# Optimization experiments

Measured on AMD Instinct MI355X. Metric: run time of the kernel, lower is better.

## Reference

```python
import jax, jax.numpy as jnp
import numpy as np

NUM_Q_HEADS = 64
NUM_KV_HEADS = 8
HEAD_DIM = 64
HIDDEN = 2880
SLIDING_WINDOW = 128
ROPE_WAVELENGTH = 10000.0
NEG_INF = jnp.float32(-1e9)


def _rope(x, start_index=0):
    # x: (b, s, n, h). yarn with scaling_factor=1.0 == standard RoPE (split-half rotate).
    s, h = x.shape[1], x.shape[-1]
    inv_freq = 1.0 / (ROPE_WAVELENGTH ** (jnp.arange(0, h, 2, dtype=jnp.float32) / h))
    pos = jnp.arange(s, dtype=jnp.float32) + start_index
    freqs = pos[:, None] * inv_freq[None, :]  # (s, h/2)
    cos = jnp.concatenate([jnp.cos(freqs), jnp.cos(freqs)], axis=-1)[None, :, None, :]
    sin = jnp.concatenate([jnp.sin(freqs), jnp.sin(freqs)], axis=-1)[None, :, None, :]
    x1, x2 = jnp.split(x, 2, axis=-1)
    rot = jnp.concatenate([-x2, x1], axis=-1)
    return x * cos + rot * sin


def setup_inputs() -> dict:
    key = jax.random.key(0)
    ks = jax.random.split(key, 9)
    b, s = 1, 2048
    scale = 0.02
    hidden_states = jax.random.normal(ks[0], (b, s, HIDDEN), jnp.float32)
    Wq = jax.random.normal(ks[1], (HIDDEN, NUM_Q_HEADS, HEAD_DIM), jnp.float32) * scale
    Wk = jax.random.normal(ks[2], (HIDDEN, NUM_KV_HEADS, HEAD_DIM), jnp.float32) * scale
    Wv = jax.random.normal(ks[3], (HIDDEN, NUM_KV_HEADS, HEAD_DIM), jnp.float32) * scale
    Wo = jax.random.normal(ks[4], (NUM_Q_HEADS, HEAD_DIM, HIDDEN), jnp.float32) * scale
    bq = jnp.zeros((NUM_Q_HEADS, HEAD_DIM), jnp.float32)
    bk = jnp.zeros((NUM_KV_HEADS, HEAD_DIM), jnp.float32)
    bv = jnp.zeros((NUM_KV_HEADS, HEAD_DIM), jnp.float32)
    bo = jnp.zeros((HIDDEN,), jnp.float32)
    sinks = jax.random.normal(ks[5], (NUM_Q_HEADS,), jnp.float32) * 0.05
    attention_mask = jnp.tril(jnp.ones((s, s), bool))[None]  # causal, (b, q, k)
    return dict(hidden_states=hidden_states, Wq=Wq, bq=bq, Wk=Wk, bk=bk, Wv=Wv,
                bv=bv, Wo=Wo, bo=bo, sinks=sinks, attention_mask=attention_mask)


def reference(hidden_states, Wq, bq, Wk, bk, Wv, bv, Wo, bo, sinks, attention_mask):
    b, s, _ = hidden_states.shape
    inv_norm = 1.0 / np.sqrt(HEAD_DIM).astype(np.float32)
    # QKV projections (EinsumDense with bias)
    q = jnp.einsum('bqm,muh->bquh', hidden_states, Wq) + bq
    k = jnp.einsum('bkm,mvh->bkvh', hidden_states, Wk) + bk
    v = jnp.einsum('bkm,mvh->bkvh', hidden_states, Wv) + bv
    # rotary_dim == head_dim (even), so RoPE applies to the full head dim
    q = _rope(q)
    k = _rope(k)
    # GQA: repeat kv heads
    groups = NUM_Q_HEADS // NUM_KV_HEADS
    k = jnp.repeat(k, groups, axis=2)
    v = jnp.repeat(v, groups, axis=2)
    scores = jnp.einsum('bquh,bkuh->buqk', q, k) * inv_norm
    # sliding-window mask: keep kv_pos >= q_pos - window
    qpos = jnp.arange(s)
    swin = qpos[None, :] >= qpos[:, None] - SLIDING_WINDOW  # (q, k)
    scores = jnp.where(swin[None, None], scores, NEG_INF)
    scores = jnp.where(attention_mask[:, None], scores, NEG_INF)
    # sink-token logit per head appended as extra kv column
    sink = jnp.broadcast_to(sinks.reshape(1, NUM_Q_HEADS, 1, 1), (b, NUM_Q_HEADS, s, 1))
    logits = jnp.concatenate([scores, sink], axis=-1)
    m = jax.lax.stop_gradient(jnp.max(logits, axis=-1, keepdims=True))
    probs = jax.nn.softmax(logits - m, axis=-1)[..., :-1]  # drop sink column
    attn = jnp.einsum('buqk,bkuh->bquh', probs, v)
    return jnp.einsum('bquh,uhm->bqm', attn, Wo) + bo
```

## Files before the change

### kernel.cpp

```cpp
#include <hip/hip_runtime.h>
#include <cstdint>

typedef __attribute__((ext_vector_type(4))) float f32x4;
typedef __attribute__((ext_vector_type(8))) short bf16x8;

#define HIDDEN 2880
#define SEQ 2048
#define QKV_N 5120
#define WIN 128

__device__ __forceinline__ ushort f2bf(float f) {
  uint32_t u = __builtin_bit_cast(uint32_t, f);
  u += 0x7fff + ((u >> 16) & 1);
  return (ushort)(u >> 16);
}
__device__ __forceinline__ float bf2f(ushort h) {
  uint32_t u = ((uint32_t)h) << 16;
  return __builtin_bit_cast(float, u);
}

__global__ void conv_kernel(const float* __restrict__ in, ushort* __restrict__ out, int n) {
  int i = (blockIdx.x * blockDim.x + threadIdx.x) * 4;
  if (i >= n) return;
  float4 v = *(const float4*)(in + i);
  ushort4 o;
  o.x = f2bf(v.x); o.y = f2bf(v.y); o.z = f2bf(v.z); o.w = f2bf(v.w);
  *(ushort4*)(out + i) = o;
}

__global__ __launch_bounds__(256) void tconv_kernel(const float* __restrict__ in, ushort* __restrict__ out,
                                                    int R, int C, int out_ld, int out_row_off) {
  __shared__ float tile[32][33];
  int c0 = blockIdx.x * 32, r0 = blockIdx.y * 32;
  int tx = threadIdx.x & 31, ty = threadIdx.x >> 5;
#pragma unroll
  for (int i = 0; i < 32; i += 8)
    tile[ty + i][tx] = in[(size_t)(r0 + ty + i) * C + c0 + tx];
  __syncthreads();
#pragma unroll
  for (int i = 0; i < 32; i += 8)
    out[(size_t)(out_row_off + c0 + ty + i) * out_ld + r0 + tx] = f2bf(tile[tx][ty + i]);
}

__global__ void biascat_kernel(const float* __restrict__ bq, const float* __restrict__ bk,
                               const float* __restrict__ bv, float* __restrict__ out) {
  int i = blockIdx.x * blockDim.x + threadIdx.x;
  if (i >= QKV_N) return;
  float v = (i < 4096) ? bq[i] : (i < 4608) ? bk[i - 4096] : bv[i - 4608];
  out[i] = v;
}

__global__ void ropetab_kernel(float2* __restrict__ tab) {
  int i = blockIdx.x * blockDim.x + threadIdx.x;
  int s = i >> 5, d = i & 31;
  float inv = powf(10000.0f, -(float)d / 32.0f);
  float f = (float)s * inv;
  tab[i] = make_float2(cosf(f), sinf(f));
}

__global__ void rope_kernel(ushort* __restrict__ buf, const float2* __restrict__ tab, int width, int total) {
  int idx = blockIdx.x * blockDim.x + threadIdx.x;
  if (idx >= total) return;
  int s = idx / width;
  int rr = idx - s * width;
  int d = rr & 63;
  ushort* p = buf + (size_t)s * QKV_N + rr;
  float x = bf2f(*p);
  float partner = __shfl_xor(x, 32, 64);
  float2 cs = tab[(s << 5) + (d & 31)];
  float o = x * cs.x + ((d < 32) ? -partner : partner) * cs.y;
  *p = f2bf(o);
}

__global__ __launch_bounds__(256) void vt_kernel(const ushort* __restrict__ qkv, ushort* __restrict__ vt) {
  __shared__ ushort tile[64][80];
  int kv0 = blockIdx.x * 64, d0 = blockIdx.y * 64;
  int t = threadIdx.x;
#pragma unroll
  for (int p = 0; p < 2; ++p) {
    int lr = p * 32 + (t >> 3);
    *(bf16x8*)&tile[lr][(t & 7) * 8] =
        *(const bf16x8*)&qkv[(size_t)(kv0 + lr) * QKV_N + 4608 + d0 + (t & 7) * 8];
  }
  __syncthreads();
#pragma unroll
  for (int p = 0; p < 2; ++p) {
    int dl = p * 32 + (t >> 3);
    bf16x8 o;
#pragma unroll
    for (int jj = 0; jj < 8; ++jj) o[jj] = (short)tile[(t & 7) * 8 + jj][dl];
    *(bf16x8*)&vt[(size_t)(d0 + dl) * 2048 + kv0 + (t & 7) * 8] = o;
  }
}

template <bool OUT_BF16>
__global__ __launch_bounds__(256, 2) void gemm4w_kernel(
    const ushort* __restrict__ A, const ushort* __restrict__ Bt,
    const float* __restrict__ bias, void* __restrict__ Cv,
    int K, int lda, int ldb, int ldc) {
  constexpr int NFRAG = 5;
  constexpr int BHALF = 160 * 64;
  constexpr int BCHUNKS = 10;
  constexpr int BUFBYTES = 16384 + 2 * BHALF;
  __shared__ __align__(16) char ldsbuf[2 * BUFBYTES];

  const int cpx = gridDim.x >> 3;
  const int wg = ((int)blockIdx.x & 7) * cpx + ((int)blockIdx.x >> 3);
  const int mtile = wg & 15, ntile = wg >> 4;
  const int m0 = mtile * 128, n0 = ntile * 160;

  const int tid = threadIdx.x, wv = tid >> 6, l = tid & 63;
  const int wm = wv >> 1, wn = wv & 1;
  const int r = l & 15, g = l >> 4;

  const int c = l ^ ((l >> 3) & 3);
  const ushort* gA0 = A + (size_t)(m0 + (c >> 2)) * lda + (c & 3) * 8;
  const ushort* gB0 = Bt + (size_t)(n0 + (c >> 2)) * ldb + (c & 3) * 8;

  const int gsw = (g * 16) ^ (((r >> 1) & 3) << 4);
  const int aOff = (wm * 64 + r) * 64 + gsw;
  const int bOff = (wn * 80 + r) * 64 + gsw;

  auto sA = [&](int nb, int kg, int kh) {
#pragma unroll
    for (int j = 0; j < 2; ++j) {
      int cid = j * 4 + wv;
      __builtin_amdgcn_global_load_lds(
          (const __attribute__((address_space(1))) void*)(const void*)(gA0 + (size_t)cid * 16 * lda + kg),
          (__attribute__((address_space(3))) void*)&ldsbuf[nb * BUFBYTES + kh * 8192 + cid * 1024], 16, 0, 0);
    }
  };
  auto sB = [&](int nb, int kg, int kh) {
#pragma unroll
    for (int j = 0; j < 3; ++j) {
      int cid = j * 4 + wv;
      if (cid < BCHUNKS)
        __builtin_amdgcn_global_load_lds(
            (const __attribute__((address_space(1))) void*)(const void*)(gB0 + (size_t)cid * 16 * ldb + kg),
            (__attribute__((address_space(3))) void*)&ldsbuf[nb * BUFBYTES + 16384 + kh * BHALF + cid * 1024],
            16, 0, 0);
    }
  };

#define BAR() __builtin_amdgcn_s_barrier()
#define LGKM0()                                              \
  do {                                                       \
    asm volatile("s_waitcnt lgkmcnt(0)" ::: "memory");       \
    __builtin_amdgcn_sched_barrier(0);                       \
  } while (0)
#define WAITV0() asm volatile("s_waitcnt vmcnt(0)" ::: "memory")

  f32x4 acc[4][NFRAG] = {};
  const int nt = K >> 6;

  sA(0, 0, 0); sA(0, 32, 1); sB(0, 0, 0); sB(0, 32, 1);
  WAITV0();
  BAR();

  for (int t = 0; t < nt; ++t) {
    const int bufOff = (t & 1) * BUFBYTES;
    const int nb = (t & 1) ^ 1;
    if (t + 1 < nt) {
      const int kn = (t + 1) * 64;
      sA(nb, kn, 0); sA(nb, kn + 32, 1);
      sB(nb, kn, 0); sB(nb, kn + 32, 1);
    }
#pragma unroll
    for (int kh = 0; kh < 2; ++kh) {
      bf16x8 aq[4], bq[NFRAG];
#pragma unroll
      for (int nf = 0; nf < NFRAG; ++nf)
        bq[nf] = *(const bf16x8*)&ldsbuf[bufOff + 16384 + kh * BHALF + bOff + nf * 1024];
#pragma unroll
      for (int mi = 0; mi < 4; ++mi)
        aq[mi] = *(const bf16x8*)&ldsbuf[bufOff + kh * 8192 + aOff + mi * 1024];
      LGKM0();
      __builtin_amdgcn_s_setprio(1);
#pragma unroll
      for (int mi = 0; mi < 4; ++mi)
#pragma unroll
        for (int nf = 0; nf < NFRAG; ++nf)
          acc[mi][nf] = __builtin_amdgcn_mfma_f32_16x16x32_bf16(aq[mi], bq[nf], acc[mi][nf], 0, 0, 0);
      __builtin_amdgcn_s_setprio(0);
    }
    WAITV0();
    BAR();
  }

#pragma unroll
  for (int mf2 = 0; mf2 < 4; ++mf2) {
#pragma unroll
    for (int nf = 0; nf < NFRAG; ++nf) {
      int cc = n0 + wn * 80 + nf * 16 + r;
      float b = bias[cc];
#pragma unroll
      for (int j = 0; j < 4; ++j) {
        int rrow = m0 + wm * 64 + mf2 * 16 + g * 4 + j;
        float v = acc[mf2][nf][j] + b;
        if (OUT_BF16) ((ushort*)Cv)[(size_t)rrow * ldc + cc] = f2bf(v);
        else ((float*)Cv)[(size_t)rrow * ldc + cc] = v;
      }
    }
  }
#undef BAR
#undef LGKM0
#undef WAITV0
}

__global__ __launch_bounds__(512, 4) void attn_kernel(
    const ushort* __restrict__ qkv, const ushort* __restrict__ vt,
    const float* __restrict__ sinks, ushort* __restrict__ out) {
  __shared__ __align__(16) char lds[54272];
  const int kh = blockIdx.y;
  const int q0 = blockIdx.x * 32;
  const int kvw0 = q0 - 128;
  const int tid = threadIdx.x, w = tid >> 6, l = tid & 63;
  const int r = l & 15, g = l >> 4;
  const int h = kh * 8 + w;

  if (tid < 256) ((uint32_t*)(lds + 40960))[tid] = 0;

#pragma unroll
  for (int it = 0; it < 3; ++it) {
    int c = it * 512 + tid;
    if (c < 1280) {
      {
        int row = c >> 3, ch = c & 7;
        int kv = kvw0 + row;
        bf16x8 vv = {};
        if (kv >= 0) vv = *(const bf16x8*)&qkv[(size_t)kv * QKV_N + 4096 + kh * 64 + ch * 8];
        int byte = (row * 128 + ch * 16) ^ ((row & 7) << 4);
        *(bf16x8*)(lds + byte) = vv;
      }
      {
        int row = c / 20, ch = c - (c / 20) * 20;
        int kv = kvw0 + ch * 8;
        bf16x8 vv = {};
        if (kv >= 0) vv = *(const bf16x8*)&vt[(size_t)(kh * 64 + row) * 2048 + kv];
        int byte = (row * 320 + ch * 16) ^ ((row & 7) << 4);
        *(bf16x8*)(lds + 20480 + byte) = vv;
      }
    }
  }
  __syncthreads();

  char* Pw = lds + 41984 + w * 1536;
  const float snk = sinks[h];

#pragma unroll
  for (int si = 0; si < 2; ++si) {
    const ushort* qb = &qkv[(size_t)(q0 + si * 16 + r) * QKV_N + h * 64 + g * 8];
    bf16x8 qf0 = *(const bf16x8*)qb;
    bf16x8 qf1 = *(const bf16x8*)(qb + 32);

    f32x4 S[9];
    float mx[4] = {-3e30f, -3e30f, -3e30f, -3e30f};
#pragma unroll
    for (int tt = 0; tt < 9; ++tt) {
      int kvloc = (si + tt) * 16 + r;
      int b0 = (kvloc * 128 + g * 16) ^ ((kvloc & 7) << 4);
      int b1 = (kvloc * 128 + 64 + g * 16) ^ ((kvloc & 7) << 4);
      bf16x8 kf0 = *(const bf16x8*)(lds + b0);
      bf16x8 kf1 = *(const bf16x8*)(lds + b1);
      f32x4 s = {};
      s = __builtin_amdgcn_mfma_f32_16x16x32_bf16(qf0, kf0, s, 0, 0, 0);
      s = __builtin_amdgcn_mfma_f32_16x16x32_bf16(qf1, kf1, s, 0, 0, 0);
      int kvc = kvw0 + kvloc;
#pragma unroll
      for (int j = 0; j < 4; ++j) {
        int qr = q0 + si * 16 + g * 4 + j;
        bool valid = (kvc >= 0) && (kvc <= qr) && (kvc >= qr - WIN);
        float v = valid ? s[j] * 0.125f : -1e30f;
        s[j] = v;
        mx[j] = fmaxf(mx[j], v);
      }
      S[tt] = s;
    }
#pragma unroll
    for (int off = 1; off < 16; off <<= 1)
#pragma unroll
      for (int j = 0; j < 4; ++j) mx[j] = fmaxf(mx[j], __shfl_xor(mx[j], off, 64));
    float m[4], sum[4] = {0, 0, 0, 0};
#pragma unroll
    for (int j = 0; j < 4; ++j) m[j] = fmaxf(mx[j], snk);
#pragma unroll
    for (int tt = 0; tt < 9; ++tt)
#pragma unroll
      for (int j = 0; j < 4; ++j) {
        float p = (S[tt][j] > -1e29f) ? __expf(S[tt][j] - m[j]) : 0.0f;
        S[tt][j] = p;
        sum[j] += p;
      }
#pragma unroll
    for (int off = 1; off < 16; off <<= 1)
#pragma unroll
      for (int j = 0; j < 4; ++j) sum[j] += __shfl_xor(sum[j], off, 64);
    float rinv[4];
#pragma unroll
    for (int j = 0; j < 4; ++j) rinv[j] = 1.0f / (sum[j] + __expf(snk - m[j]));

    f32x4 acc[4] = {};
#pragma unroll
    for (int ks = 0; ks < 5; ++ks) {
#pragma unroll
      for (int c2 = 0; c2 < 2; ++c2) {
        int tt = 2 * ks + c2;
#pragma unroll
        for (int j = 0; j < 4; ++j) {
          float pv = (tt <= 8) ? S[tt][j] * rinv[j] : 0.0f;
          *(ushort*)(Pw + ((g * 4 + j) * 48 + c2 * 16 + r) * 2) = f2bf(pv);
        }
      }
      bf16x8 pa = *(const bf16x8*)(Pw + (r * 48 + g * 8) * 2);
#pragma unroll
      for (int ni = 0; ni < 4; ++ni) {
        int row = ni * 16 + r;
        int byte = (row * 320 + (si * 16 + ks * 32 + g * 8) * 2) ^ ((row & 7) << 4);
        bf16x8 vb = *(const bf16x8*)(lds + 20480 + byte);
        acc[ni] = __builtin_amdgcn_mfma_f32_16x16x32_bf16(pa, vb, acc[ni], 0, 0, 0);
      }
    }
#pragma unroll
    for (int ni = 0; ni < 4; ++ni)
#pragma unroll
      for (int j = 0; j < 4; ++j)
        out[(size_t)(q0 + si * 16 + g * 4 + j) * 4096 + h * 64 + ni * 16 + r] = f2bf(acc[ni][j]);
  }
}

extern "C" void kernel_launch(void* const* d_in, const int* in_sizes, int n_in,
                              void* d_out, int out_size, void* d_ws, size_t ws_size,
                              hipStream_t stream) {
  const float* hs = (const float*)d_in[0];
  const float* Wq = (const float*)d_in[1];
  const float* bq = (const float*)d_in[2];
  const float* Wk = (const float*)d_in[3];
  const float* bk = (const float*)d_in[4];
  const float* Wv = (const float*)d_in[5];
  const float* bv = (const float*)d_in[6];
  const float* Wo = (const float*)d_in[7];
  const float* bo = (const float*)d_in[8];
  const float* sinks = (const float*)d_in[9];
  float* out = (float*)d_out;

  char* ws = (char*)d_ws;
  ushort* hs_bf   = (ushort*)(ws + 0);
  ushort* vt_g    = (ushort*)(ws + 0);
  ushort* wqkv_t  = (ushort*)(ws + 11796480);
  ushort* attn    = (ushort*)(ws + 11796480);
  ushort* wo_t    = (ushort*)(ws + 41287680);
  ushort* qkv     = (ushort*)(ws + 66453504);
  float*  bias_all= (float*)(ws + 87425024);
  float2* tab     = (float2*)(ws + 87445504);

  conv_kernel<<<5898240 / 4 / 256, 256, 0, stream>>>(hs, hs_bf, 5898240);
  tconv_kernel<<<dim3(4096 / 32, 2880 / 32), 256, 0, stream>>>(Wq, wqkv_t, 2880, 4096, 2880, 0);
  tconv_kernel<<<dim3(512 / 32, 2880 / 32), 256, 0, stream>>>(Wk, wqkv_t, 2880, 512, 2880, 4096);
  tconv_kernel<<<dim3(512 / 32, 2880 / 32), 256, 0, stream>>>(Wv, wqkv_t, 2880, 512, 2880, 4608);
  tconv_kernel<<<dim3(2880 / 32, 4096 / 32), 256, 0, stream>>>(Wo, wo_t, 4096, 2880, 4096, 0);
  biascat_kernel<<<20, 256, 0, stream>>>(bq, bk, bv, bias_all);
  ropetab_kernel<<<2048 * 32 / 256, 256, 0, stream>>>(tab);

  gemm4w_kernel<true><<<512, 256, 0, stream>>>(hs_bf, wqkv_t, bias_all, qkv,
                                               2880, 2880, 2880, 5120);
  rope_kernel<<<8388608 / 256, 256, 0, stream>>>(qkv, tab, 4096, 8388608);
  rope_kernel<<<1048576 / 256, 256, 0, stream>>>(qkv + 4096, tab, 512, 1048576);
  vt_kernel<<<dim3(32, 8), 256, 0, stream>>>(qkv, vt_g);
  attn_kernel<<<dim3(64, 8), 512, 0, stream>>>(qkv, vt_g, sinks, attn);
  gemm4w_kernel<false><<<288, 256, 0, stream>>>(attn, wo_t, bo, out,
                                                4096, 4096, 4096, 2880);
}
```

Measured before the change: 219.6 us.

## Split GEMM prefetch per K-half with partial vmcnt waits, vectorize RoPE

```diff
diff --git a/kernel.cpp b/kernel.cpp
--- a/kernel.cpp
+++ b/kernel.cpp
@@ -58,18 +58,26 @@
   tab[i] = make_float2(cosf(f), sinf(f));
 }
 
-__global__ void rope_kernel(ushort* __restrict__ buf, const float2* __restrict__ tab, int width, int total) {
+__global__ void rope8_kernel(ushort* __restrict__ buf, const float2* __restrict__ tab,
+                             int perrow , int total) {
   int idx = blockIdx.x * blockDim.x + threadIdx.x;
   if (idx >= total) return;
-  int s = idx / width;
-  int rr = idx - s * width;
-  int d = rr & 63;
-  ushort* p = buf + (size_t)s * QKV_N + rr;
-  float x = bf2f(*p);
-  float partner = __shfl_xor(x, 32, 64);
-  float2 cs = tab[(s << 5) + (d & 31)];
-  float o = x * cs.x + ((d < 32) ? -partner : partner) * cs.y;
-  *p = f2bf(o);
+  int s = idx / perrow;
+  int p = idx - s * perrow;
+  int head = p >> 2, j = p & 2 * 2 - 1;
+  ushort* base = buf + (size_t)s * QKV_N + head * 64 + j * 8;
+  bf16x8 x1 = *(const bf16x8*)base;
+  bf16x8 x2 = *(const bf16x8*)(base + 32);
+  bf16x8 o1, o2;
+#pragma unroll
+  for (int i = 0; i < 8; ++i) {
+    float2 cs = tab[(s << 5) + j * 8 + i];
+    float a = bf2f((ushort)x1[i]), b = bf2f((ushort)x2[i]);
+    o1[i] = (short)f2bf(a * cs.x - b * cs.y);
+    o2[i] = (short)f2bf(b * cs.x + a * cs.y);
+  }
+  *(bf16x8*)base = o1;
+  *(bf16x8*)(base + 32) = o2;
 }
 
 __global__ __launch_bounds__(256) void vt_kernel(const ushort* __restrict__ qkv, ushort* __restrict__ vt) {
@@ -93,21 +101,24 @@
   }
 }
 
-template <bool OUT_BF16>
-__global__ __launch_bounds__(256, 2) void gemm4w_kernel(
+template <int BN, bool OUT_BF16>
+__global__ __launch_bounds__(256, 2) void gemm2p_kernel(
     const ushort* __restrict__ A, const ushort* __restrict__ Bt,
     const float* __restrict__ bias, void* __restrict__ Cv,
     int K, int lda, int ldb, int ldc) {
-  constexpr int NFRAG = 5;
-  constexpr int BHALF = 160 * 64;
-  constexpr int BCHUNKS = 10;
+  constexpr int NFRAG = BN / 32;
+  constexpr int BHALF = BN * 64;
+  constexpr int BCHUNKS = BHALF / 1024;
+  static_assert(BCHUNKS % 4 == 2, "per-wave vmcnt immediates assume BCHUNKS%4==2");
+  constexpr int WHI = 2 + (BCHUNKS + 3) / 4;
+  constexpr int WLO = 2 + (BCHUNKS + 1) / 4;
   constexpr int BUFBYTES = 16384 + 2 * BHALF;
   __shared__ __align__(16) char ldsbuf[2 * BUFBYTES];
 
   const int cpx = gridDim.x >> 3;
   const int wg = ((int)blockIdx.x & 7) * cpx + ((int)blockIdx.x >> 3);
   const int mtile = wg & 15, ntile = wg >> 4;
-  const int m0 = mtile * 128, n0 = ntile * 160;
+  const int m0 = mtile * 128, n0 = ntile * BN;
 
   const int tid = threadIdx.x, wv = tid >> 6, l = tid & 63;
   const int wm = wv >> 1, wn = wv & 1;
@@ -119,7 +130,7 @@
 
   const int gsw = (g * 16) ^ (((r >> 1) & 3) << 4);
   const int aOff = (wm * 64 + r) * 64 + gsw;
-  const int bOff = (wn * 80 + r) * 64 + gsw;
+  const int bOff = (wn * (NFRAG * 16) + r) * 64 + gsw;
 
   auto sA = [&](int nb, int kg, int kh) {
 #pragma unroll
@@ -132,7 +143,7 @@
   };
   auto sB = [&](int nb, int kg, int kh) {
 #pragma unroll
-    for (int j = 0; j < 3; ++j) {
+    for (int j = 0; j < (BCHUNKS + 3) / 4; ++j) {
       int cid = j * 4 + wv;
       if (cid < BCHUNKS)
         __builtin_amdgcn_global_load_lds(
@@ -142,29 +153,31 @@
     }
   };
 
-#define BAR() __builtin_amdgcn_s_barrier()
-#define LGKM0()                                              \
-  do {                                                       \
-    asm volatile("s_waitcnt lgkmcnt(0)" ::: "memory");       \
-    __builtin_amdgcn_sched_barrier(0);                       \
+#define BARRIER_PIN()                         \
+  do {                                        \
+    __builtin_amdgcn_s_barrier();             \
+    __builtin_amdgcn_sched_barrier(0);        \
   } while (0)
-#define WAITV0() asm volatile("s_waitcnt vmcnt(0)" ::: "memory")
+#define WAITN()                                                                     \
+  do {                                                                              \
+    if (wv < 2) asm volatile("s_waitcnt vmcnt(%0)" ::"n"(WHI) : "memory");          \
+    else asm volatile("s_waitcnt vmcnt(%0)" ::"n"(WLO) : "memory");                 \
+  } while (0)
+#define WAIT0() asm volatile("s_waitcnt vmcnt(0)" ::: "memory")
 
   f32x4 acc[4][NFRAG] = {};
   const int nt = K >> 6;
 
-  sA(0, 0, 0); sA(0, 32, 1); sB(0, 0, 0); sB(0, 32, 1);
-  WAITV0();
-  BAR();
+  sA(0, 0, 0); sB(0, 0, 0);
+  sA(0, 32, 1); sB(0, 32, 1);
+  WAITN();
+  BARRIER_PIN();
 
   for (int t = 0; t < nt; ++t) {
     const int bufOff = (t & 1) * BUFBYTES;
     const int nb = (t & 1) ^ 1;
-    if (t + 1 < nt) {
-      const int kn = (t + 1) * 64;
-      sA(nb, kn, 0); sA(nb, kn + 32, 1);
-      sB(nb, kn, 0); sB(nb, kn + 32, 1);
-    }
+    const int kn = (t + 1) << 6;
+    const bool more = (t + 1 < nt);
 #pragma unroll
     for (int kh = 0; kh < 2; ++kh) {
       bf16x8 aq[4], bq[NFRAG];
@@ -174,7 +187,7 @@
 #pragma unroll
       for (int mi = 0; mi < 4; ++mi)
         aq[mi] = *(const bf16x8*)&ldsbuf[bufOff + kh * 8192 + aOff + mi * 1024];
-      LGKM0();
+      if (more) { sA(nb, kn + kh * 32, kh); sB(nb, kn + kh * 32, kh); }
       __builtin_amdgcn_s_setprio(1);
 #pragma unroll
       for (int mi = 0; mi < 4; ++mi)
@@ -182,16 +195,16 @@
         for (int nf = 0; nf < NFRAG; ++nf)
           acc[mi][nf] = __builtin_amdgcn_mfma_f32_16x16x32_bf16(aq[mi], bq[nf], acc[mi][nf], 0, 0, 0);
       __builtin_amdgcn_s_setprio(0);
-    }
-    WAITV0();
-    BAR();
+      if (more) WAITN(); else WAIT0();
+      BARRIER_PIN();
+    }
   }
 
 #pragma unroll
   for (int mf2 = 0; mf2 < 4; ++mf2) {
 #pragma unroll
     for (int nf = 0; nf < NFRAG; ++nf) {
-      int cc = n0 + wn * 80 + nf * 16 + r;
+      int cc = n0 + wn * (NFRAG * 16) + nf * 16 + r;
       float b = bias[cc];
 #pragma unroll
       for (int j = 0; j < 4; ++j) {
@@ -202,9 +215,9 @@
       }
     }
   }
-#undef BAR
-#undef LGKM0
-#undef WAITV0
+#undef BARRIER_PIN
+#undef WAITN
+#undef WAIT0
 }
 
 __global__ __launch_bounds__(512, 4) void attn_kernel(
@@ -361,12 +374,12 @@
   biascat_kernel<<<20, 256, 0, stream>>>(bq, bk, bv, bias_all);
   ropetab_kernel<<<2048 * 32 / 256, 256, 0, stream>>>(tab);
 
-  gemm4w_kernel<true><<<512, 256, 0, stream>>>(hs_bf, wqkv_t, bias_all, qkv,
-                                               2880, 2880, 2880, 5120);
-  rope_kernel<<<8388608 / 256, 256, 0, stream>>>(qkv, tab, 4096, 8388608);
-  rope_kernel<<<1048576 / 256, 256, 0, stream>>>(qkv + 4096, tab, 512, 1048576);
+  gemm2p_kernel<160, true><<<512, 256, 0, stream>>>(hs_bf, wqkv_t, bias_all, qkv,
+                                                    2880, 2880, 2880, 5120);
+  rope8_kernel<<<2048, 256, 0, stream>>>(qkv, tab, 256, 2048 * 256);
+  rope8_kernel<<<256, 256, 0, stream>>>(qkv + 4096, tab, 32, 2048 * 32);
   vt_kernel<<<dim3(32, 8), 256, 0, stream>>>(qkv, vt_g);
   attn_kernel<<<dim3(64, 8), 512, 0, stream>>>(qkv, vt_g, sinks, attn);
-  gemm4w_kernel<false><<<288, 256, 0, stream>>>(attn, wo_t, bo, out,
-                                                4096, 4096, 4096, 2880);
-}
+  gemm2p_kernel<96, false><<<480, 256, 0, stream>>>(attn, wo_t, bo, out,
+                                                    4096, 4096, 4096, 2880);
+}
```

Result: faster. 211.7 us (-3.6%).

## Fuse RoPE into QKV GEMM epilogue with head-aligned 128-wide N tiles

Applied to the files above, without the earlier changes.

```diff
diff --git a/kernel.cpp b/kernel.cpp
--- a/kernel.cpp
+++ b/kernel.cpp
@@ -58,20 +58,6 @@
   tab[i] = make_float2(cosf(f), sinf(f));
 }
 
-__global__ void rope_kernel(ushort* __restrict__ buf, const float2* __restrict__ tab, int width, int total) {
-  int idx = blockIdx.x * blockDim.x + threadIdx.x;
-  if (idx >= total) return;
-  int s = idx / width;
-  int rr = idx - s * width;
-  int d = rr & 63;
-  ushort* p = buf + (size_t)s * QKV_N + rr;
-  float x = bf2f(*p);
-  float partner = __shfl_xor(x, 32, 64);
-  float2 cs = tab[(s << 5) + (d & 31)];
-  float o = x * cs.x + ((d < 32) ? -partner : partner) * cs.y;
-  *p = f2bf(o);
-}
-
 __global__ __launch_bounds__(256) void vt_kernel(const ushort* __restrict__ qkv, ushort* __restrict__ vt) {
   __shared__ ushort tile[64][80];
   int kv0 = blockIdx.x * 64, d0 = blockIdx.y * 64;
@@ -93,21 +79,22 @@
   }
 }
 
-template <bool OUT_BF16>
+template <int BN, bool OUT_BF16, bool ROPE>
 __global__ __launch_bounds__(256, 2) void gemm4w_kernel(
     const ushort* __restrict__ A, const ushort* __restrict__ Bt,
-    const float* __restrict__ bias, void* __restrict__ Cv,
-    int K, int lda, int ldb, int ldc) {
-  constexpr int NFRAG = 5;
-  constexpr int BHALF = 160 * 64;
-  constexpr int BCHUNKS = 10;
+    const float* __restrict__ bias, const float2* __restrict__ tab,
+    void* __restrict__ Cv, int K, int lda, int ldb, int ldc) {
+  constexpr int NFRAG = BN / 32;
+  constexpr int BHALF = BN * 64;
+  constexpr int BCHUNKS = BHALF / 1024;
   constexpr int BUFBYTES = 16384 + 2 * BHALF;
+  static_assert(!ROPE || NFRAG == 4, "RoPE fusion requires BN=128");
   __shared__ __align__(16) char ldsbuf[2 * BUFBYTES];
 
   const int cpx = gridDim.x >> 3;
   const int wg = ((int)blockIdx.x & 7) * cpx + ((int)blockIdx.x >> 3);
   const int mtile = wg & 15, ntile = wg >> 4;
-  const int m0 = mtile * 128, n0 = ntile * 160;
+  const int m0 = mtile * 128, n0 = ntile * BN;
 
   const int tid = threadIdx.x, wv = tid >> 6, l = tid & 63;
   const int wm = wv >> 1, wn = wv & 1;
@@ -119,7 +106,7 @@
 
   const int gsw = (g * 16) ^ (((r >> 1) & 3) << 4);
   const int aOff = (wm * 64 + r) * 64 + gsw;
-  const int bOff = (wn * 80 + r) * 64 + gsw;
+  const int bOff = (wn * (NFRAG * 16) + r) * 64 + gsw;
 
   auto sA = [&](int nb, int kg, int kh) {
 #pragma unroll
@@ -132,7 +119,7 @@
   };
   auto sB = [&](int nb, int kg, int kh) {
 #pragma unroll
-    for (int j = 0; j < 3; ++j) {
+    for (int j = 0; j < (BCHUNKS + 3) / 4; ++j) {
       int cid = j * 4 + wv;
       if (cid < BCHUNKS)
         __builtin_amdgcn_global_load_lds(
@@ -187,18 +174,40 @@
     BAR();
   }
 
+  const bool doRope = ROPE && (n0 < 4608);
 #pragma unroll
   for (int mf2 = 0; mf2 < 4; ++mf2) {
+    float vb[NFRAG][4];
 #pragma unroll
     for (int nf = 0; nf < NFRAG; ++nf) {
-      int cc = n0 + wn * 80 + nf * 16 + r;
+      int cc = n0 + wn * (NFRAG * 16) + nf * 16 + r;
       float b = bias[cc];
+#pragma unroll
+      for (int j = 0; j < 4; ++j) vb[nf][j] = acc[mf2][nf][j] + b;
+    }
+    if constexpr (ROPE) {
+      if (doRope) {
+#pragma unroll
+        for (int j = 0; j < 4; ++j) {
+          int s = m0 + wm * 64 + mf2 * 16 + g * 4 + j;
+          float2 cs0 = tab[(s << 5) + r];
+          float2 cs1 = tab[(s << 5) + 16 + r];
+          float q0 = vb[0][j] * cs0.x - vb[2][j] * cs0.y;
+          float q1 = vb[1][j] * cs1.x - vb[3][j] * cs1.y;
+          float q2 = vb[2][j] * cs0.x + vb[0][j] * cs0.y;
+          float q3 = vb[3][j] * cs1.x + vb[1][j] * cs1.y;
+          vb[0][j] = q0; vb[1][j] = q1; vb[2][j] = q2; vb[3][j] = q3;
+        }
+      }
+    }
+#pragma unroll
+    for (int nf = 0; nf < NFRAG; ++nf) {
+      int cc = n0 + wn * (NFRAG * 16) + nf * 16 + r;
 #pragma unroll
       for (int j = 0; j < 4; ++j) {
         int rrow = m0 + wm * 64 + mf2 * 16 + g * 4 + j;
-        float v = acc[mf2][nf][j] + b;
-        if (OUT_BF16) ((ushort*)Cv)[(size_t)rrow * ldc + cc] = f2bf(v);
-        else ((float*)Cv)[(size_t)rrow * ldc + cc] = v;
+        if (OUT_BF16) ((ushort*)Cv)[(size_t)rrow * ldc + cc] = f2bf(vb[nf][j]);
+        else ((float*)Cv)[(size_t)rrow * ldc + cc] = vb[nf][j];
       }
     }
   }
@@ -361,12 +370,10 @@
   biascat_kernel<<<20, 256, 0, stream>>>(bq, bk, bv, bias_all);
   ropetab_kernel<<<2048 * 32 / 256, 256, 0, stream>>>(tab);
 
-  gemm4w_kernel<true><<<512, 256, 0, stream>>>(hs_bf, wqkv_t, bias_all, qkv,
-                                               2880, 2880, 2880, 5120);
-  rope_kernel<<<8388608 / 256, 256, 0, stream>>>(qkv, tab, 4096, 8388608);
-  rope_kernel<<<1048576 / 256, 256, 0, stream>>>(qkv + 4096, tab, 512, 1048576);
+  gemm4w_kernel<128, true, true><<<640, 256, 0, stream>>>(hs_bf, wqkv_t, bias_all, tab, qkv,
+                                                          2880, 2880, 2880, 5120);
   vt_kernel<<<dim3(32, 8), 256, 0, stream>>>(qkv, vt_g);
   attn_kernel<<<dim3(64, 8), 512, 0, stream>>>(qkv, vt_g, sinks, attn);
-  gemm4w_kernel<false><<<288, 256, 0, stream>>>(attn, wo_t, bo, out,
-                                                4096, 4096, 4096, 2880);
-}
+  gemm4w_kernel<160, false, false><<<288, 256, 0, stream>>>(attn, wo_t, bo, tab, out,
+                                                            4096, 4096, 4096, 2880);
+}
```

After: 226.7 us. 1.03x slower.
